# Kernel optimization log

Measured on AMD Instinct MI355X. Metric: run time of the kernel, lower is better.

Reference implementation:

```python
import jax, jax.numpy as jnp
import numpy as np

B, N, M, D = 256, 256, 256, 4
PID_MAX = 5

def setup_inputs() -> dict:
    key = jax.random.key(0)
    k1, k2, k3, k4 = jax.random.split(key, 4)
    return {
        "target": jax.random.normal(k1, (B, N, D), dtype=jnp.float32),
        "reco": jax.random.normal(k2, (B, M, D), dtype=jnp.float32),
        "in_pid": jax.random.randint(k3, (B, N), 0, PID_MAX),
        "out_pid": jax.random.randint(k4, (B, M), 0, PID_MAX),
    }

def reference(target, reco, in_pid, out_pid):
    dt = target.dtype
    mask_x = in_pid != 0   # [B, N] valid (non-zero-pid) target particles
    mask_y = out_pid != 0  # [B, M] valid reco particles
    fx = mask_x.astype(dt)
    fy = mask_y.astype(dt)
    n_in = jnp.maximum(jnp.asarray(1.0, dt), fx.sum(-1))    # [B]
    n_out = jnp.maximum(jnp.asarray(1.0, dt), fy.sum(-1))   # [B]

    # pairwise Euclidean distances between valid points; invalid pairs -> +inf
    diff = target[:, :, None, :] - reco[:, None, :, :]       # [B, N, M, D]
    dist = jnp.sqrt(jnp.sum(diff * diff, axis=-1))           # [B, N, M]
    pair_mask = mask_x[:, :, None] & mask_y[:, None, :]
    dist_m = jnp.where(pair_mask, dist, jnp.inf)

    min_xy = jnp.min(dist_m, axis=-1)                        # [B, N] nearest reco per target
    min_yx = jnp.min(dist_m, axis=-2)                        # [B, M] nearest target per reco
    sum_xy = jnp.sum(jnp.where(mask_x, min_xy, 0.0), axis=-1)
    sum_yx = jnp.sum(jnp.where(mask_y, min_yx, 0.0), axis=-1)
    normal = 0.5 * (sum_xy / n_out + sum_yx / n_in)          # [B]

    # edge cases matching the torch branches:
    # if no valid reco: sum ||x_nonzero|| / n_in ; elif no valid target: 0
    x_norms = jnp.linalg.norm(target, axis=-1)               # [B, N]
    fallback = jnp.sum(jnp.where(mask_x, x_norms, 0.0), axis=-1) / n_in
    has_x = mask_x.any(-1)
    has_y = mask_y.any(-1)
    per_nonzero = jnp.where(~has_y, fallback,
                            jnp.where(~has_x, jnp.asarray(0.0, dt), normal))

    # zero-pid reco particles: mean norm (denominator clamped to >=1)
    y_norms = jnp.linalg.norm(reco, axis=-1)                 # [B, M]
    n_y_zero = jnp.maximum(jnp.asarray(1.0, dt), (1.0 - fy).sum(-1))
    per_zero = jnp.sum(jnp.where(~mask_y, y_norms, 0.0), axis=-1) / n_y_zero

    eucl_non_zero = jnp.mean(per_nonzero)
    eucl_zero = jnp.mean(per_zero)
    return (eucl_non_zero, eucl_zero)
```

## Files before the change

kernel.cpp:

```cpp
#include <hip/hip_runtime.h>
#include <math.h>

#define B_ 256
#define N_ 256
#define M_ 256

__device__ inline float wave_sum(float v) {
    v += __shfl_down(v, 32, 64);
    v += __shfl_down(v, 16, 64);
    v += __shfl_down(v, 8, 64);
    v += __shfl_down(v, 4, 64);
    v += __shfl_down(v, 2, 64);
    v += __shfl_down(v, 1, 64);
    return v;
}

__device__ inline float dist2(const float4 a, const float4 r) {
    const float dx = a.x - r.x;
    const float dy = a.y - r.y;
    const float dz = a.z - r.z;
    const float dw = a.w - r.w;
    return fmaf(dx, dx, fmaf(dy, dy, fmaf(dz, dz, dw * dw)));
}

__global__ __launch_bounds__(1024, 4) void chamfer_full_kernel(
    const float4* __restrict__ target,
    const float4* __restrict__ reco,
    const int*    __restrict__ in_pid,
    const int*    __restrict__ out_pid,
    float*        __restrict__ out)
{
    const int b = blockIdx.x;
    const int t = threadIdx.x;

    __shared__ float4 s_t[N_];
    __shared__ float4 s_r[M_];
    __shared__ float  s_mx[N_];
    __shared__ float  s_my[M_];
    __shared__ float  partials[16][6];

    const float SENT = 1e18f;

    float c_fx = 0.f, c_fy = 0.f, c_xn = 0.f, c_yz = 0.f;
    if (t < N_) {
        const float4 v = target[b * N_ + t];
        const bool m = (in_pid[b * N_ + t] != 0);
        s_t[t]  = m ? v : make_float4(SENT, SENT, SENT, SENT);
        s_mx[t] = m ? 1.f : 0.f;
        if (m) {
            c_fx = 1.f;
            c_xn = sqrtf(fmaf(v.x, v.x, fmaf(v.y, v.y, fmaf(v.z, v.z, v.w * v.w))));
        }
    } else if (t < N_ + M_) {
        const int r = t - N_;
        const float4 v = reco[b * M_ + r];
        const bool m = (out_pid[b * M_ + r] != 0);
        s_r[r]  = m ? v : make_float4(SENT, SENT, SENT, SENT);
        s_my[r] = m ? 1.f : 0.f;
        if (m) {
            c_fy = 1.f;
        } else {
            c_yz = sqrtf(fmaf(v.x, v.x, fmaf(v.y, v.y, fmaf(v.z, v.z, v.w * v.w))));
        }
    }
    __syncthreads();

    const int c   = t & 15;
    const int g   = t >> 4;
    const int row = g * 4;

    const float4 a0 = s_t[row + 0];
    const float4 a1 = s_t[row + 1];
    const float4 a2 = s_t[row + 2];
    const float4 a3 = s_t[row + 3];
    float am0 = 3.0e38f, am1 = 3.0e38f, am2 = 3.0e38f, am3 = 3.0e38f;
    #pragma unroll
    for (int i = 0; i < 16; ++i) {
        const float4 r = s_r[i * 16 + c];
        am0 = fminf(am0, dist2(a0, r));
        am1 = fminf(am1, dist2(a1, r));
        am2 = fminf(am2, dist2(a2, r));
        am3 = fminf(am3, dist2(a3, r));
    }
    #pragma unroll
    for (int off = 8; off >= 1; off >>= 1) {
        am0 = fminf(am0, __shfl_xor(am0, off, 64));
        am1 = fminf(am1, __shfl_xor(am1, off, 64));
        am2 = fminf(am2, __shfl_xor(am2, off, 64));
        am3 = fminf(am3, __shfl_xor(am3, off, 64));
    }
    float c_sxy = 0.f;
    if (c == 0) {
        c_sxy = s_mx[row + 0] * sqrtf(am0) + s_mx[row + 1] * sqrtf(am1)
              + s_mx[row + 2] * sqrtf(am2) + s_mx[row + 3] * sqrtf(am3);
    }

    const float4 b0 = s_r[row + 0];
    const float4 b1 = s_r[row + 1];
    const float4 b2 = s_r[row + 2];
    const float4 b3 = s_r[row + 3];
    float bm0 = 3.0e38f, bm1 = 3.0e38f, bm2 = 3.0e38f, bm3 = 3.0e38f;
    #pragma unroll
    for (int i = 0; i < 16; ++i) {
        const float4 q = s_t[i * 16 + c];
        bm0 = fminf(bm0, dist2(b0, q));
        bm1 = fminf(bm1, dist2(b1, q));
        bm2 = fminf(bm2, dist2(b2, q));
        bm3 = fminf(bm3, dist2(b3, q));
    }
    #pragma unroll
    for (int off = 8; off >= 1; off >>= 1) {
        bm0 = fminf(bm0, __shfl_xor(bm0, off, 64));
        bm1 = fminf(bm1, __shfl_xor(bm1, off, 64));
        bm2 = fminf(bm2, __shfl_xor(bm2, off, 64));
        bm3 = fminf(bm3, __shfl_xor(bm3, off, 64));
    }
    float c_syx = 0.f;
    if (c == 0) {
        c_syx = s_my[row + 0] * sqrtf(bm0) + s_my[row + 1] * sqrtf(bm1)
              + s_my[row + 2] * sqrtf(bm2) + s_my[row + 3] * sqrtf(bm3);
    }

    const int wave = t >> 6;
    const int lane = t & 63;
    const float r0 = wave_sum(c_sxy);
    const float r1 = wave_sum(c_syx);
    const float r2 = wave_sum(c_fx);
    const float r3 = wave_sum(c_fy);
    const float r4 = wave_sum(c_xn);
    const float r5 = wave_sum(c_yz);
    if (lane == 0) {
        partials[wave][0] = r0;
        partials[wave][1] = r1;
        partials[wave][2] = r2;
        partials[wave][3] = r3;
        partials[wave][4] = r4;
        partials[wave][5] = r5;
    }
    __syncthreads();

    if (t == 0) {
        float sxy = 0.f, syx = 0.f, fx = 0.f, fy = 0.f, xn = 0.f, yz = 0.f;
        #pragma unroll
        for (int w = 0; w < 16; ++w) {
            sxy += partials[w][0];
            syx += partials[w][1];
            fx  += partials[w][2];
            fy  += partials[w][3];
            xn  += partials[w][4];
            yz  += partials[w][5];
        }
        const float n_in   = fmaxf(1.0f, fx);
        const float n_out  = fmaxf(1.0f, fy);
        const bool  has_x  = (fx > 0.0f);
        const bool  has_y  = (fy > 0.0f);
        const float normal   = 0.5f * (sxy / n_out + syx / n_in);
        const float fallback = xn / n_in;
        const float per_nz   = (!has_y) ? fallback : ((!has_x) ? 0.0f : normal);
        const float n_y_zero = fmaxf(1.0f, (float)M_ - fy);
        const float per_z    = yz / n_y_zero;

        atomicAdd(&out[0], per_nz * (1.0f / (float)B_));
        atomicAdd(&out[1], per_z  * (1.0f / (float)B_));
    }
}

extern "C" void kernel_launch(void* const* d_in, const int* in_sizes, int n_in,
                              void* d_out, int out_size, void* d_ws, size_t ws_size,
                              hipStream_t stream) {
    const float4* target  = (const float4*)d_in[0];
    const float4* reco    = (const float4*)d_in[1];
    const int*    in_pid  = (const int*)d_in[2];
    const int*    out_pid = (const int*)d_in[3];
    float*        out     = (float*)d_out;

    hipMemsetAsync(out, 0, (size_t)out_size * sizeof(float), stream);
    chamfer_full_kernel<<<B_, 1024, 0, stream>>>(target, reco, in_pid, out_pid, out);
}
```

Before: 75.57 us.

## Compute column minima in the row pass via shared-memory atomicMin

After: 72.77 us. 3.7% less time.

```diff
diff --git a/kernel.cpp b/kernel.cpp
--- a/kernel.cpp
+++ b/kernel.cpp
@@ -33,11 +33,12 @@
     const int b = blockIdx.x;
     const int t = threadIdx.x;
 
-    __shared__ float4 s_t[N_];
-    __shared__ float4 s_r[M_];
-    __shared__ float  s_mx[N_];
-    __shared__ float  s_my[M_];
-    __shared__ float  partials[16][6];
+    __shared__ float4   s_t[N_];
+    __shared__ float4   s_r[M_];
+    __shared__ float    s_mx[N_];
+    __shared__ float    s_my[M_];
+    __shared__ unsigned s_colmin[M_];
+    __shared__ float4   partials[16];
 
     const float SENT = 1e18f;
 
@@ -62,6 +63,8 @@
         } else {
             c_yz = sqrtf(fmaf(v.x, v.x, fmaf(v.y, v.y, fmaf(v.z, v.z, v.w * v.w))));
         }
+    } else if (t < N_ + M_ + M_) {
+        s_colmin[t - (N_ + M_)] = 0x7F7FFFFFu;
     }
     __syncthreads();
 
@@ -74,14 +77,27 @@
     const float4 a2 = s_t[row + 2];
     const float4 a3 = s_t[row + 3];
     float am0 = 3.0e38f, am1 = 3.0e38f, am2 = 3.0e38f, am3 = 3.0e38f;
+
     #pragma unroll
     for (int i = 0; i < 16; ++i) {
-        const float4 r = s_r[i * 16 + c];
-        am0 = fminf(am0, dist2(a0, r));
-        am1 = fminf(am1, dist2(a1, r));
-        am2 = fminf(am2, dist2(a2, r));
-        am3 = fminf(am3, dist2(a3, r));
+        const int m = i * 16 + c;
+        const float4 r = s_r[m];
+        const float d0 = dist2(a0, r);
+        const float d1 = dist2(a1, r);
+        const float d2_ = dist2(a2, r);
+        const float d3 = dist2(a3, r);
+        am0 = fminf(am0, d0);
+        am1 = fminf(am1, d1);
+        am2 = fminf(am2, d2_);
+        am3 = fminf(am3, d3);
+        float cmin = fminf(fminf(d0, d1), fminf(d2_, d3));
+        cmin = fminf(cmin, __shfl_xor(cmin, 16, 64));
+        cmin = fminf(cmin, __shfl_xor(cmin, 32, 64));
+        if ((t & 48) == 0) {
+            atomicMin(&s_colmin[m], __float_as_uint(cmin));
+        }
     }
+
     #pragma unroll
     for (int off = 8; off >= 1; off >>= 1) {
         am0 = fminf(am0, __shfl_xor(am0, off, 64));
@@ -94,67 +110,43 @@
         c_sxy = s_mx[row + 0] * sqrtf(am0) + s_mx[row + 1] * sqrtf(am1)
               + s_mx[row + 2] * sqrtf(am2) + s_mx[row + 3] * sqrtf(am3);
     }
+    __syncthreads();
 
-    const float4 b0 = s_r[row + 0];
-    const float4 b1 = s_r[row + 1];
-    const float4 b2 = s_r[row + 2];
-    const float4 b3 = s_r[row + 3];
-    float bm0 = 3.0e38f, bm1 = 3.0e38f, bm2 = 3.0e38f, bm3 = 3.0e38f;
-    #pragma unroll
-    for (int i = 0; i < 16; ++i) {
-        const float4 q = s_t[i * 16 + c];
-        bm0 = fminf(bm0, dist2(b0, q));
-        bm1 = fminf(bm1, dist2(b1, q));
-        bm2 = fminf(bm2, dist2(b2, q));
-        bm3 = fminf(bm3, dist2(b3, q));
-    }
-    #pragma unroll
-    for (int off = 8; off >= 1; off >>= 1) {
-        bm0 = fminf(bm0, __shfl_xor(bm0, off, 64));
-        bm1 = fminf(bm1, __shfl_xor(bm1, off, 64));
-        bm2 = fminf(bm2, __shfl_xor(bm2, off, 64));
-        bm3 = fminf(bm3, __shfl_xor(bm3, off, 64));
-    }
     float c_syx = 0.f;
-    if (c == 0) {
-        c_syx = s_my[row + 0] * sqrtf(bm0) + s_my[row + 1] * sqrtf(bm1)
-              + s_my[row + 2] * sqrtf(bm2) + s_my[row + 3] * sqrtf(bm3);
+    if (t >= N_ && t < N_ + M_) {
+        const int m = t - N_;
+        c_syx = s_my[m] * sqrtf(__uint_as_float(s_colmin[m]));
     }
 
+    float sxy = c_sxy;
+    sxy += __shfl_xor(sxy, 16, 64);
+    sxy += __shfl_xor(sxy, 32, 64);
     const int wave = t >> 6;
     const int lane = t & 63;
-    const float r0 = wave_sum(c_sxy);
-    const float r1 = wave_sum(c_syx);
-    const float r2 = wave_sum(c_fx);
-    const float r3 = wave_sum(c_fy);
-    const float r4 = wave_sum(c_xn);
-    const float r5 = wave_sum(c_yz);
-    if (lane == 0) {
-        partials[wave][0] = r0;
-        partials[wave][1] = r1;
-        partials[wave][2] = r2;
-        partials[wave][3] = r3;
-        partials[wave][4] = r4;
-        partials[wave][5] = r5;
-    }
+    float v0 = (wave < 4) ? c_fx : c_fy;
+    float v1 = (wave < 4) ? c_xn : c_yz;
+    float v2 = c_syx;
+    v0 = wave_sum(v0);
+    v1 = wave_sum(v1);
+    v2 = wave_sum(v2);
+    if (lane == 0) partials[wave] = make_float4(sxy, v0, v1, v2);
     __syncthreads();
 
     if (t == 0) {
-        float sxy = 0.f, syx = 0.f, fx = 0.f, fy = 0.f, xn = 0.f, yz = 0.f;
+        float sxy_t = 0.f, syx_t = 0.f, fx = 0.f, fy = 0.f, xn = 0.f, yz = 0.f;
         #pragma unroll
         for (int w = 0; w < 16; ++w) {
-            sxy += partials[w][0];
-            syx += partials[w][1];
-            fx  += partials[w][2];
-            fy  += partials[w][3];
-            xn  += partials[w][4];
-            yz  += partials[w][5];
+            const float4 p = partials[w];
+            sxy_t += p.x;
+            syx_t += p.w;
+            if (w < 4)      { fx += p.y; xn += p.z; }
+            else if (w < 8) { fy += p.y; yz += p.z; }
         }
         const float n_in   = fmaxf(1.0f, fx);
         const float n_out  = fmaxf(1.0f, fy);
         const bool  has_x  = (fx > 0.0f);
         const bool  has_y  = (fy > 0.0f);
-        const float normal   = 0.5f * (sxy / n_out + syx / n_in);
+        const float normal   = 0.5f * (sxy_t / n_out + syx_t / n_in);
         const float fallback = xn / n_in;
         const float per_nz   = (!has_y) ? fallback : ((!has_x) ? 0.0f : normal);
         const float n_y_zero = fmaxf(1.0f, (float)M_ - fy);
```
